# Kernel optimization log

Hardware: AMD Instinct MI355X
Metric: run time of the kernel (lower is better)

The kernel has to match this reference:

```python
import jax, jax.numpy as jnp
import numpy as np

D_MODEL = 1024
NUM_HEADS = 16
D_K = D_MODEL // NUM_HEADS

def setup_inputs() -> dict:
    key = jax.random.key(0)
    ks = jax.random.split(key, 8)
    B, S, D = 2, 2048, D_MODEL
    scale = 1.0 / np.sqrt(D)
    return {
        "X_q": jax.random.normal(ks[0], (B, S, D), dtype=jnp.float32),
        "X_k": jax.random.normal(ks[1], (B, S, D), dtype=jnp.float32),
        "X_v": jax.random.normal(ks[2], (B, S, D), dtype=jnp.float32),
        "W_q": jax.random.normal(ks[3], (D, D), dtype=jnp.float32) * scale,
        "W_k": jax.random.normal(ks[4], (D, D), dtype=jnp.float32) * scale,
        "W_v": jax.random.normal(ks[5], (D, D), dtype=jnp.float32) * scale,
        "W_o": jax.random.normal(ks[6], (D, D), dtype=jnp.float32) * scale,
        "b_o": jnp.zeros((D,), dtype=jnp.float32),
    }

def reference(X_q, X_k, X_v, W_q, W_k, W_v, W_o, b_o):
    B, S, D = X_q.shape
    H, dk = NUM_HEADS, D_K
    # nn.Linear: x @ W.T
    Q = (X_q @ W_q.T).reshape(B, H, S, dk)  # faithful raw view, no transpose
    K = (X_k @ W_k.T).reshape(B, H, S, dk)
    V = (X_v @ W_v.T).reshape(B, H, S, dk)
    A = jnp.einsum("bhqd,bhkd->bhqk", Q, K) / np.sqrt(dk)  # [B,H,S,S]
    A = jax.nn.softmax(A, axis=-1)
    H_cat = jnp.einsum("bhqk,bhkd->bhqd", A, V).reshape(B, S, D)
    return H_cat @ W_o.T + b_o
```

## Files before the change

kernel.cpp:

```cpp
#include <hip/hip_runtime.h>

typedef __bf16 bf16;
typedef bf16 bf16x8 __attribute__((ext_vector_type(8)));
typedef bf16 bf16x4 __attribute__((ext_vector_type(4)));
typedef bf16 bf16x2 __attribute__((ext_vector_type(2)));
typedef float f32x4 __attribute__((ext_vector_type(4)));
typedef float f32x16 __attribute__((ext_vector_type(16)));
typedef int i32x4 __attribute__((ext_vector_type(4)));

#define XSZ 4194304
#define WSZ 1048576
#define KDIM 1024
#define QSCALE 0.1803368801111137f

__device__ __forceinline__ void async16(const bf16* g, bf16* l) {
  __builtin_amdgcn_global_load_lds(
      (const __attribute__((address_space(1))) unsigned int*)g,
      (__attribute__((address_space(3))) unsigned int*)l, 16, 0, 0);
}

__device__ __forceinline__ bf16x8 ld16(const bf16* p) {
  return __builtin_bit_cast(bf16x8, *(const i32x4*)p);
}

__device__ __forceinline__ f32x4 mfma16(bf16x8 a, bf16x8 b, f32x4 c) {
  return __builtin_amdgcn_mfma_f32_16x16x32_bf16(a, b, c, 0, 0, 0);
}
__device__ __forceinline__ f32x16 mfma32(bf16x8 a, bf16x8 b, f32x16 c) {
  return __builtin_amdgcn_mfma_f32_32x32x16_bf16(a, b, c, 0, 0, 0);
}

__device__ __forceinline__ int packbf2(float lo, float hi) {
  bf16x2 t; t[0] = (bf16)lo; t[1] = (bf16)hi;
  return __builtin_bit_cast(int, t);
}

__device__ __forceinline__ float fast_exp2(float x) {
#if __has_builtin(__builtin_amdgcn_exp2f)
  return __builtin_amdgcn_exp2f(x);
#else
  return exp2f(x);
#endif
}


__global__ __launch_bounds__(256) void cast_all(const float* __restrict__ Xq, const float* __restrict__ Xk,
                                                const float* __restrict__ Xv, const float* __restrict__ Wq,
                                                const float* __restrict__ Wk, const float* __restrict__ Wv,
                                                const float* __restrict__ Wo, bf16* __restrict__ dst) {
  size_t i = ((size_t)blockIdx.x * 256 + threadIdx.x) * 8;
  const float* src; size_t off; float scale = 1.0f;
  if (i < XSZ)                { src = Xq; off = i; }
  else if (i < 2 * (size_t)XSZ) { src = Xk; off = i - XSZ; }
  else if (i < 3 * (size_t)XSZ) { src = Xv; off = i - 2 * (size_t)XSZ; }
  else if (i < 3 * (size_t)XSZ + WSZ) { src = Wq; off = i - 3 * (size_t)XSZ; scale = QSCALE; }
  else if (i < 3 * (size_t)XSZ + 2 * (size_t)WSZ) { src = Wk; off = i - 3 * (size_t)XSZ - WSZ; }
  else if (i < 3 * (size_t)XSZ + 3 * (size_t)WSZ) { src = Wv; off = i - 3 * (size_t)XSZ - 2 * (size_t)WSZ; }
  else                        { src = Wo; off = i - 3 * (size_t)XSZ - 3 * (size_t)WSZ; }
  float4 a = *(const float4*)(src + off);
  float4 b = *(const float4*)(src + off + 4);
  bf16x8 o;
  o[0] = (bf16)(a.x * scale); o[1] = (bf16)(a.y * scale);
  o[2] = (bf16)(a.z * scale); o[3] = (bf16)(a.w * scale);
  o[4] = (bf16)(b.x * scale); o[5] = (bf16)(b.y * scale);
  o[6] = (bf16)(b.z * scale); o[7] = (bf16)(b.w * scale);
  *(bf16x8*)(dst + i) = o;
}

__device__ __forceinline__ void gemm_nt_core(const bf16* __restrict__ A, const bf16* __restrict__ Bm,
                                             int m0, int n0, bf16* lds, f32x4 acc[4][4]) {
  const int t = threadIdx.x;
  const int lane = t & 63, wave = t >> 6;
  const int wm = wave & 1, wn = wave >> 1;
  const int quad = lane >> 4, m16 = lane & 15;
  bf16* As = lds;
  bf16* Bs = lds + 128 * 64;
  const bf16* gA[4]; int dstc[4];
  #pragma unroll
  for (int j = 0; j < 4; j++) {
    int c = t + j * 256;
    int row = c >> 3;
    int col = ((c & 7) ^ (row & 7)) * 8;
    gA[j] = A + (size_t)(m0 + row) * KDIM + col;
    dstc[j] = c * 8;
  }
  const ptrdiff_t dBA = (Bm + (size_t)n0 * KDIM) - (A + (size_t)m0 * KDIM);
  const int swz = (m16 & 7) * 8;
  for (int kt = 0; kt < KDIM; kt += 64) {
    #pragma unroll
    for (int j = 0; j < 4; j++) async16(gA[j] + kt, As + dstc[j]);
    #pragma unroll
    for (int j = 0; j < 4; j++) async16(gA[j] + dBA + kt, Bs + dstc[j]);
    __syncthreads();
    #pragma unroll
    for (int s = 0; s < 2; s++) {
      bf16x8 af[4], bfv[4];
      #pragma unroll
      for (int i = 0; i < 4; i++)
        af[i] = ld16(As + (wm * 64 + i * 16 + m16) * 64 + ((s * 32 + quad * 8) ^ swz));
      #pragma unroll
      for (int i = 0; i < 4; i++)
        bfv[i] = ld16(Bs + (wn * 64 + i * 16 + m16) * 64 + ((s * 32 + quad * 8) ^ swz));
      #pragma unroll
      for (int mi = 0; mi < 4; mi++)
        #pragma unroll
        for (int ni = 0; ni < 4; ni++)
          acc[mi][ni] = mfma16(af[mi], bfv[ni], acc[mi][ni]);
    }
    __syncthreads();
  }
}

__global__ __launch_bounds__(256, 3) void proj_gemm(const bf16* __restrict__ xq, const bf16* __restrict__ xk,
                                                 const bf16* __restrict__ xv, const bf16* __restrict__ wq,
                                                 const bf16* __restrict__ wk, const bf16* __restrict__ wv,
                                                 bf16* __restrict__ Qo, bf16* __restrict__ Ko,
                                                 bf16* __restrict__ Vo) {
  __shared__ __align__(16) bf16 lds[2 * 128 * 64];
  const int z = blockIdx.z;
  const bf16* A = (z == 0) ? xq : (z == 1) ? xk : xv;
  const bf16* W = (z == 0) ? wq : (z == 1) ? wk : wv;
  bf16* C = (z == 0) ? Qo : (z == 1) ? Ko : Vo;
  f32x4 acc[4][4];
  #pragma unroll
  for (int i = 0; i < 4; i++)
    #pragma unroll
    for (int j = 0; j < 4; j++) acc[i][j] = (f32x4){0.f, 0.f, 0.f, 0.f};
  gemm_nt_core(A, W, blockIdx.y * 128, blockIdx.x * 128, lds, acc);
  const int lane = threadIdx.x & 63, wave = threadIdx.x >> 6;
  const int wm = wave & 1, wn = wave >> 1, quad = lane >> 4, m16 = lane & 15;
  const int row0 = blockIdx.y * 128 + wm * 64;
  const int col0 = blockIdx.x * 128 + wn * 64;
  #pragma unroll
  for (int mi = 0; mi < 4; mi++)
    #pragma unroll
    for (int ni = 0; ni < 4; ni++)
      #pragma unroll
      for (int r = 0; r < 4; r++) {
        int row = row0 + mi * 16 + quad * 4 + r;
        int col = col0 + ni * 16 + m16;
        C[(size_t)row * 1024 + col] = (bf16)acc[mi][ni][r];
      }
}

__global__ __launch_bounds__(256, 3) void out_gemm(const bf16* __restrict__ Hm, const bf16* __restrict__ wo,
                                                const float* __restrict__ bias, float* __restrict__ out) {
  __shared__ __align__(16) bf16 lds[128 * 64 + 64 * 64];
  bf16* As = lds;
  bf16* Bs = lds + 128 * 64;
  const int t = threadIdx.x;
  const int lane = t & 63, wave = t >> 6;
  const int wm = wave & 1, wn = wave >> 1;
  const int quad = lane >> 4, m16 = lane & 15;
  const int m0 = blockIdx.y * 128, n0 = blockIdx.x * 64;
  const bf16* gA[4]; int dstA[4];
  #pragma unroll
  for (int j = 0; j < 4; j++) {
    int c = t + j * 256;
    int row = c >> 3;
    int col = ((c & 7) ^ (row & 7)) * 8;
    gA[j] = Hm + (size_t)(m0 + row) * KDIM + col;
    dstA[j] = c * 8;
  }
  const bf16* gB[2]; int dstB[2];
  #pragma unroll
  for (int j = 0; j < 2; j++) {
    int c = t + j * 256;
    int row = c >> 3;
    int col = ((c & 7) ^ (row & 7)) * 8;
    gB[j] = wo + (size_t)(n0 + row) * KDIM + col;
    dstB[j] = c * 8;
  }
  const int swz = (m16 & 7) * 8;
  f32x4 acc[4][2];
  #pragma unroll
  for (int i = 0; i < 4; i++)
    #pragma unroll
    for (int j = 0; j < 2; j++) acc[i][j] = (f32x4){0.f, 0.f, 0.f, 0.f};
  for (int kt = 0; kt < KDIM; kt += 64) {
    #pragma unroll
    for (int j = 0; j < 4; j++) async16(gA[j] + kt, As + dstA[j]);
    #pragma unroll
    for (int j = 0; j < 2; j++) async16(gB[j] + kt, Bs + dstB[j]);
    __syncthreads();
    #pragma unroll
    for (int s = 0; s < 2; s++) {
      bf16x8 af[4], bfv[2];
      #pragma unroll
      for (int i = 0; i < 4; i++)
        af[i] = ld16(As + (wm * 64 + i * 16 + m16) * 64 + ((s * 32 + quad * 8) ^ swz));
      #pragma unroll
      for (int i = 0; i < 2; i++)
        bfv[i] = ld16(Bs + (wn * 32 + i * 16 + m16) * 64 + ((s * 32 + quad * 8) ^ swz));
      #pragma unroll
      for (int mi = 0; mi < 4; mi++)
        #pragma unroll
        for (int ni = 0; ni < 2; ni++)
          acc[mi][ni] = mfma16(af[mi], bfv[ni], acc[mi][ni]);
    }
    __syncthreads();
  }
  const int row0 = m0 + wm * 64;
  const int col0 = n0 + wn * 32;
  float bv[2];
  #pragma unroll
  for (int ni = 0; ni < 2; ni++) bv[ni] = bias[col0 + ni * 16 + m16];
  #pragma unroll
  for (int mi = 0; mi < 4; mi++)
    #pragma unroll
    for (int ni = 0; ni < 2; ni++)
      #pragma unroll
      for (int r = 0; r < 4; r++) {
        int row = row0 + mi * 16 + quad * 4 + r;
        int col = col0 + ni * 16 + m16;
        out[(size_t)row * 1024 + col] = acc[mi][ni][r] + bv[ni];
      }
}

__global__ __launch_bounds__(256) void transpose_v(const bf16* __restrict__ V, bf16* __restrict__ Vt) {
  __shared__ bf16 T[64 * 65];
  const int t = threadIdx.x;
  const bf16* src = V + (size_t)blockIdx.y * (2048 * 64) + (size_t)blockIdx.x * 64 * 64;
  bf16* dst = Vt + (size_t)blockIdx.y * (2048 * 64) + (size_t)blockIdx.x * 64;
  #pragma unroll
  for (int j = 0; j < 2; j++) {
    int c = t + j * 256;
    int row = c >> 3, col8 = (c & 7) * 8;
    bf16x8 v = *(const bf16x8*)(src + row * 64 + col8);
    #pragma unroll
    for (int i = 0; i < 8; i++) T[row * 65 + col8 + i] = v[i];
  }
  __syncthreads();
  #pragma unroll
  for (int j = 0; j < 2; j++) {
    int c = t + j * 256;
    int d = c >> 3, k8 = (c & 7) * 8;
    bf16x8 o;
    #pragma unroll
    for (int i = 0; i < 8; i++) o[i] = T[(k8 + i) * 65 + d];
    *(bf16x8*)(dst + (size_t)d * 2048 + k8) = o;
  }
}

__global__ __launch_bounds__(512, 2) void attn_kernel(const bf16* __restrict__ Qg,
                                                      const bf16* __restrict__ Kg,
                                                      const bf16* __restrict__ Vtg,
                                                      bf16* __restrict__ Hout) {
  __shared__ __align__(16) bf16 smem[32768];
  const int t = threadIdx.x;
  const int lane = t & 63;
  const int w = (t >> 6) & 3;
  const int half = t >> 8;
  const int tt = t & 255;
  const int l31 = lane & 31, h = lane >> 5, l7 = lane & 7;
  bf16* hb = smem + half * 16384;
  const int L = blockIdx.x + 16 * blockIdx.y;
  const int xcd = L & 7, j5 = L >> 3;
  const int bh = xcd * 4 + (j5 & 3);
  const int qt = j5 >> 2;
  const size_t base = (size_t)bh * (2048 * 64);
  const bf16* Kp = Kg + base;
  const bf16* Vp = Vtg + base;
  const int q = qt * 128 + w * 32 + l31;

  bf16x8 qf[4];
  #pragma unroll
  for (int kc = 0; kc < 4; kc++)
    qf[kc] = *(const bf16x8*)(Qg + base + (size_t)q * 64 + 16 * kc + 8 * h);

  f32x16 oacc[2];
  #pragma unroll
  for (int mt = 0; mt < 2; mt++)
    #pragma unroll
    for (int i = 0; i < 16; i++) oacc[mt][i] = 0.f;
  float lrow = 0.f;

  const bf16* ksrc[2]; const bf16* vsrc[2]; int dstc[2];
  #pragma unroll
  for (int j = 0; j < 2; j++) {
    int c = tt + j * 256;
    int row = c >> 3;
    int sw = ((c & 7) ^ (row & 7)) * 8;
    ksrc[j] = Kp + (size_t)(half * 1024 + row) * 64 + sw;
    vsrc[j] = Vp + (size_t)row * 2048 + half * 1024 + sw;
    dstc[j] = c * 8;
  }

  #pragma unroll
  for (int j = 0; j < 2; j++) {
    async16(ksrc[j], hb + dstc[j]);
    async16(vsrc[j], hb + 4096 + dstc[j]);
  }

  for (int st = 0; st < 16; ++st) {
    __syncthreads();
    const int buf = st & 1;
    if (st + 1 < 16) {
      const int nb = (buf ^ 1) * 8192;
      #pragma unroll
      for (int j = 0; j < 2; j++) {
        async16(ksrc[j] + (st + 1) * 4096, hb + nb + dstc[j]);
        async16(vsrc[j] + (st + 1) * 64,   hb + nb + 4096 + dstc[j]);
      }
    }
    bf16* Kb = hb + buf * 8192;
    bf16* Vb = Kb + 4096;

    #pragma unroll
    for (int mtq = 0; mtq < 2; mtq++) {
      f32x16 sacc;
      #pragma unroll
      for (int i = 0; i < 16; i++) sacc[i] = 0.f;
      #pragma unroll
      for (int kc = 0; kc < 4; kc++) {
        bf16x8 kf = ld16(Kb + (32 * mtq + l31) * 64 + (((2 * kc + h) ^ l7) << 3));
        sacc = mfma32(kf, qf[kc], sacc);
      }
      int pd[8];
      float sum = 0.f;
      #pragma unroll
      for (int p = 0; p < 8; p++) {
        float p0 = fast_exp2(sacc[2 * p]);
        float p1 = fast_exp2(sacc[2 * p + 1]);
        sum += p0 + p1;
        pd[p] = packbf2(p0, p1);
      }
      lrow += sum;
      #pragma unroll
      for (int c1 = 0; c1 < 2; c1++) {
        const int kcp = 2 * mtq + c1;
        const int rro = 2 * c1 + h;
        const int rrp = 2 * c1 + 1 - h;
        int s0 = __shfl_xor(pd[2 * rrp], 32, 64);
        int s1 = __shfl_xor(pd[2 * rrp + 1], 32, 64);
        int o0 = pd[2 * rro], o1 = pd[2 * rro + 1];
        i32x4 w4;
        w4.x = h ? s0 : o0;
        w4.y = h ? s1 : o1;
        w4.z = h ? o0 : s0;
        w4.w = h ? o1 : s1;
        bf16x8 pfrag = __builtin_bit_cast(bf16x8, w4);
        #pragma unroll
        for (int mtd = 0; mtd < 2; mtd++) {
          bf16x8 vf = ld16(Vb + (32 * mtd + l31) * 64 + (((2 * kcp + h) ^ l7) << 3));
          oacc[mtd] = mfma32(vf, pfrag, oacc[mtd]);
        }
      }
    }
  }
  __syncthreads();

  lrow += __shfl_xor(lrow, 32, 64);
  float* Sf = (float*)smem;
  float* Tf = Sf + w * 2048;
  float* Lb = Sf + 8192 + w * 32;
  if (half) {
    #pragma unroll
    for (int mt = 0; mt < 2; mt++)
      #pragma unroll
      for (int r = 0; r < 16; r++) {
        int d = 32 * mt + (r & 3) + 8 * (r >> 2) + 4 * h;
        Tf[d * 32 + l31] = oacc[mt][r];
      }
    if (!h) Lb[l31] = lrow;
  }
  __syncthreads();
  if (!half) {
    float linv = 1.f / (lrow + Lb[l31]);
    #pragma unroll
    for (int mt = 0; mt < 2; mt++)
      #pragma unroll
      for (int r = 0; r < 16; r++) {
        int d = 32 * mt + (r & 3) + 8 * (r >> 2) + 4 * h;
        Tf[d * 32 + l31] = (oacc[mt][r] + Tf[d * 32 + l31]) * linv;
      }
  }
  __syncthreads();
  bf16* Hq = Hout + base + (size_t)(qt * 128 + w * 32 + l31) * 64 + 32 * h;
  #pragma unroll
  for (int s = 0; s < 2; s++) {
    int se = half * 2 + s;
    bf16x8 o;
    #pragma unroll
    for (int i = 0; i < 8; i++) o[i] = (bf16)Tf[(32 * h + se * 8 + i) * 32 + l31];
    *(bf16x8*)(Hq + se * 8) = o;
  }
}

extern "C" void kernel_launch(void* const* d_in, const int* in_sizes, int n_in,
                              void* d_out, int out_size, void* d_ws, size_t ws_size,
                              hipStream_t stream) {
  const float* Xq = (const float*)d_in[0];
  const float* Xk = (const float*)d_in[1];
  const float* Xv = (const float*)d_in[2];
  const float* Wq = (const float*)d_in[3];
  const float* Wk = (const float*)d_in[4];
  const float* Wv = (const float*)d_in[5];
  const float* Wo = (const float*)d_in[6];
  const float* bo = (const float*)d_in[7];

  bf16* ws = (bf16*)d_ws;
  bf16* xq = ws;
  bf16* xk = ws + XSZ;
  bf16* xv = ws + 2 * (size_t)XSZ;
  bf16* wq = ws + 3 * (size_t)XSZ;
  bf16* wk = wq + WSZ;
  bf16* wv = wk + WSZ;
  bf16* wo = wv + WSZ;
  bf16* q  = wo + WSZ;
  bf16* k  = q + XSZ;
  bf16* v  = k + XSZ;
  bf16* vt = xv;
  bf16* h  = xq;

  cast_all<<<8192, 256, 0, stream>>>(Xq, Xk, Xv, Wq, Wk, Wv, Wo, ws);
  proj_gemm<<<dim3(8, 32, 3), 256, 0, stream>>>(xq, xk, xv, wq, wk, wv, q, k, v);
  transpose_v<<<dim3(32, 32), 256, 0, stream>>>(v, vt);
  attn_kernel<<<dim3(16, 32), 512, 0, stream>>>(q, k, vt, h);
  out_gemm<<<dim3(16, 32), 256, 0, stream>>>(h, wo, bo, (float*)d_out);
}
```

Measured before the change: 238.3 us.

## Double-buffer LDS tiles with BK=32 prefetch in projection and output GEMMs

Both the QKV projection GEMM and the output GEMM switch from a single-buffered BK=64 loop with two barriers per iteration to a double-buffered BK=32 loop. The next tile's async global-to-LDS loads are issued before the current tile's MFMA work, with one barrier per iteration. This is meant to overlap memory latency with compute. In exchange it doubles the iteration count, halves the MFMA work per barrier, and changes the LDS swizzle to a 4-chunk pattern that may raise bank conflicts.

```diff
diff --git a/kernel.cpp b/kernel.cpp
--- a/kernel.cpp
+++ b/kernel.cpp
@@ -73,41 +73,47 @@
   const int lane = t & 63, wave = t >> 6;
   const int wm = wave & 1, wn = wave >> 1;
   const int quad = lane >> 4, m16 = lane & 15;
-  bf16* As = lds;
-  bf16* Bs = lds + 128 * 64;
-  const bf16* gA[4]; int dstc[4];
-  #pragma unroll
-  for (int j = 0; j < 4; j++) {
+  const bf16* gA[2]; int dstc[2];
+  #pragma unroll
+  for (int j = 0; j < 2; j++) {
     int c = t + j * 256;
-    int row = c >> 3;
-    int col = ((c & 7) ^ (row & 7)) * 8;
+    int row = c >> 2;
+    int col = ((c & 3) ^ (row & 3)) * 8;
     gA[j] = A + (size_t)(m0 + row) * KDIM + col;
     dstc[j] = c * 8;
   }
   const ptrdiff_t dBA = (Bm + (size_t)n0 * KDIM) - (A + (size_t)m0 * KDIM);
-  const int swz = (m16 & 7) * 8;
-  for (int kt = 0; kt < KDIM; kt += 64) {
-    #pragma unroll
-    for (int j = 0; j < 4; j++) async16(gA[j] + kt, As + dstc[j]);
-    #pragma unroll
-    for (int j = 0; j < 4; j++) async16(gA[j] + dBA + kt, Bs + dstc[j]);
+  const int swzA = quad ^ (m16 & 3);
+  #pragma unroll
+  for (int j = 0; j < 2; j++) {
+    async16(gA[j], lds + dstc[j]);
+    async16(gA[j] + dBA, lds + 4096 + dstc[j]);
+  }
+  for (int kt = 0; kt < 32; ++kt) {
     __syncthreads();
-    #pragma unroll
-    for (int s = 0; s < 2; s++) {
-      bf16x8 af[4], bfv[4];
-      #pragma unroll
-      for (int i = 0; i < 4; i++)
-        af[i] = ld16(As + (wm * 64 + i * 16 + m16) * 64 + ((s * 32 + quad * 8) ^ swz));
-      #pragma unroll
-      for (int i = 0; i < 4; i++)
-        bfv[i] = ld16(Bs + (wn * 64 + i * 16 + m16) * 64 + ((s * 32 + quad * 8) ^ swz));
-      #pragma unroll
-      for (int mi = 0; mi < 4; mi++)
-        #pragma unroll
-        for (int ni = 0; ni < 4; ni++)
-          acc[mi][ni] = mfma16(af[mi], bfv[ni], acc[mi][ni]);
+    const int cur = (kt & 1) * 8192;
+    if (kt + 1 < 32) {
+      const int nxt = 8192 - cur;
+      #pragma unroll
+      for (int j = 0; j < 2; j++) {
+        async16(gA[j] + (kt + 1) * 32, lds + nxt + dstc[j]);
+        async16(gA[j] + dBA + (kt + 1) * 32, lds + nxt + 4096 + dstc[j]);
+      }
     }
-    __syncthreads();
+    const bf16* As = lds + cur;
+    const bf16* Bs = As + 4096;
+    bf16x8 af[4], bfv[4];
+    #pragma unroll
+    for (int i = 0; i < 4; i++)
+      af[i] = ld16(As + (wm * 64 + i * 16 + m16) * 32 + swzA * 8);
+    #pragma unroll
+    for (int i = 0; i < 4; i++)
+      bfv[i] = ld16(Bs + (wn * 64 + i * 16 + m16) * 32 + swzA * 8);
+    #pragma unroll
+    for (int mi = 0; mi < 4; mi++)
+      #pragma unroll
+      for (int ni = 0; ni < 4; ni++)
+        acc[mi][ni] = mfma16(af[mi], bfv[ni], acc[mi][ni]);
   }
 }
 
@@ -116,7 +122,7 @@
                                                  const bf16* __restrict__ wk, const bf16* __restrict__ wv,
                                                  bf16* __restrict__ Qo, bf16* __restrict__ Ko,
                                                  bf16* __restrict__ Vo) {
-  __shared__ __align__(16) bf16 lds[2 * 128 * 64];
+  __shared__ __align__(16) bf16 lds[2 * 8192];
   const int z = blockIdx.z;
   const bf16* A = (z == 0) ? xq : (z == 1) ? xk : xv;
   const bf16* W = (z == 0) ? wq : (z == 1) ? wk : wv;
@@ -145,60 +151,61 @@
 
 __global__ __launch_bounds__(256, 3) void out_gemm(const bf16* __restrict__ Hm, const bf16* __restrict__ wo,
                                                 const float* __restrict__ bias, float* __restrict__ out) {
-  __shared__ __align__(16) bf16 lds[128 * 64 + 64 * 64];
-  bf16* As = lds;
-  bf16* Bs = lds + 128 * 64;
+  __shared__ __align__(16) bf16 lds[2 * 6144];
   const int t = threadIdx.x;
   const int lane = t & 63, wave = t >> 6;
   const int wm = wave & 1, wn = wave >> 1;
   const int quad = lane >> 4, m16 = lane & 15;
   const int m0 = blockIdx.y * 128, n0 = blockIdx.x * 64;
-  const bf16* gA[4]; int dstA[4];
-  #pragma unroll
-  for (int j = 0; j < 4; j++) {
+  const bf16* gA[2]; int dstA[2];
+  #pragma unroll
+  for (int j = 0; j < 2; j++) {
     int c = t + j * 256;
-    int row = c >> 3;
-    int col = ((c & 7) ^ (row & 7)) * 8;
+    int row = c >> 2;
+    int col = ((c & 3) ^ (row & 3)) * 8;
     gA[j] = Hm + (size_t)(m0 + row) * KDIM + col;
     dstA[j] = c * 8;
   }
-  const bf16* gB[2]; int dstB[2];
-  #pragma unroll
-  for (int j = 0; j < 2; j++) {
-    int c = t + j * 256;
-    int row = c >> 3;
-    int col = ((c & 7) ^ (row & 7)) * 8;
-    gB[j] = wo + (size_t)(n0 + row) * KDIM + col;
-    dstB[j] = c * 8;
-  }
-  const int swz = (m16 & 7) * 8;
+  const bf16* gB; int dstB;
+  {
+    int c = t;
+    int row = c >> 2;
+    int col = ((c & 3) ^ (row & 3)) * 8;
+    gB = wo + (size_t)(n0 + row) * KDIM + col;
+    dstB = c * 8;
+  }
+  const int swzA = quad ^ (m16 & 3);
   f32x4 acc[4][2];
   #pragma unroll
   for (int i = 0; i < 4; i++)
     #pragma unroll
     for (int j = 0; j < 2; j++) acc[i][j] = (f32x4){0.f, 0.f, 0.f, 0.f};
-  for (int kt = 0; kt < KDIM; kt += 64) {
-    #pragma unroll
-    for (int j = 0; j < 4; j++) async16(gA[j] + kt, As + dstA[j]);
-    #pragma unroll
-    for (int j = 0; j < 2; j++) async16(gB[j] + kt, Bs + dstB[j]);
+  #pragma unroll
+  for (int j = 0; j < 2; j++) async16(gA[j], lds + dstA[j]);
+  async16(gB, lds + 4096 + dstB);
+  for (int kt = 0; kt < 32; ++kt) {
     __syncthreads();
-    #pragma unroll
-    for (int s = 0; s < 2; s++) {
-      bf16x8 af[4], bfv[2];
-      #pragma unroll
-      for (int i = 0; i < 4; i++)
-        af[i] = ld16(As + (wm * 64 + i * 16 + m16) * 64 + ((s * 32 + quad * 8) ^ swz));
-      #pragma unroll
-      for (int i = 0; i < 2; i++)
-        bfv[i] = ld16(Bs + (wn * 32 + i * 16 + m16) * 64 + ((s * 32 + quad * 8) ^ swz));
-      #pragma unroll
-      for (int mi = 0; mi < 4; mi++)
-        #pragma unroll
-        for (int ni = 0; ni < 2; ni++)
-          acc[mi][ni] = mfma16(af[mi], bfv[ni], acc[mi][ni]);
+    const int cur = (kt & 1) * 6144;
+    if (kt + 1 < 32) {
+      const int nxt = 6144 - cur;
+      #pragma unroll
+      for (int j = 0; j < 2; j++) async16(gA[j] + (kt + 1) * 32, lds + nxt + dstA[j]);
+      async16(gB + (kt + 1) * 32, lds + nxt + 4096 + dstB);
     }
-    __syncthreads();
+    const bf16* As = lds + cur;
+    const bf16* Bs = As + 4096;
+    bf16x8 af[4], bfv[2];
+    #pragma unroll
+    for (int i = 0; i < 4; i++)
+      af[i] = ld16(As + (wm * 64 + i * 16 + m16) * 32 + swzA * 8);
+    #pragma unroll
+    for (int i = 0; i < 2; i++)
+      bfv[i] = ld16(Bs + (wn * 32 + i * 16 + m16) * 32 + swzA * 8);
+    #pragma unroll
+    for (int mi = 0; mi < 4; mi++)
+      #pragma unroll
+      for (int ni = 0; ni < 2; ni++)
+        acc[mi][ni] = mfma16(af[mi], bfv[ni], acc[mi][ni]);
   }
   const int row0 = m0 + wm * 64;
   const int col0 = n0 + wn * 32;
```

Result: faster. 230.8 us (-3.1%).
